# Kernel tuning notes

Hardware: AMD Instinct MI355X
Metric: run time of the kernel (lower is better)

Reference implementation:

```python
import jax, jax.numpy as jnp
import numpy as np

PS = 7        # pooled_size == conved_size
IMG = 300     # img_size
FMAP = 19     # feature map spatial size
SMAX = IMG // 16  # clamp max (18), matches torch long clamp(0, 300/16)
EPS = 1e-5


def _bn(x, g, b, m, v):
    scale = (g * jax.lax.rsqrt(v + EPS))[None, :, None, None]
    return x * scale + (b - m * g * jax.lax.rsqrt(v + EPS))[None, :, None, None]


def _conv(x, W, b=None, pad=1):
    y = jax.lax.conv_general_dilated(x, W, (1, 1), [(pad, pad), (pad, pad)],
                                     dimension_numbers=('NCHW', 'OIHW', 'NCHW'))
    if b is not None:
        y = y + b[None, :, None, None]
    return y


def _adaptive_w(lo, hi):
    # Per-ROI adaptive-avg-pool weights over the full 19-wide axis.
    # lo, hi: [B,R] inclusive crop bounds. Returns [B,R,PS,FMAP].
    H = hi - lo + 1                                  # crop length per ROI
    i = jnp.arange(PS)
    s = (i[None, None, :] * H[..., None]) // PS      # bin start (floor)
    e = -((-(i[None, None, :] + 1) * H[..., None]) // PS)  # bin end (ceil)
    rows = jnp.arange(FMAP)
    start = lo[..., None, None] + s[..., None]
    stop = lo[..., None, None] + e[..., None]
    mask = (rows >= start) & (rows < stop)
    denom = jnp.maximum(e - s, 1).astype(jnp.float32)[..., None]
    return mask.astype(jnp.float32) / denom


def setup_inputs() -> dict:
    key = jax.random.key(0)
    ks = jax.random.split(key, 6)
    B, R = 8, 128
    return {
        'roi_proposal': jax.random.uniform(ks[0], (B, 1, R, 5), dtype=jnp.float32),
        'features': jax.random.normal(ks[1], (B, 1024, FMAP, FMAP), dtype=jnp.float32),
        'W1': jax.random.normal(ks[2], (256, 1024, 3, 3), dtype=jnp.float32) * 0.02,
        'b1': jnp.zeros((256,), jnp.float32),
        'g1': jnp.ones((256,), jnp.float32),
        'be1': jnp.zeros((256,), jnp.float32),
        'm1': jnp.zeros((256,), jnp.float32),
        'v1': jnp.ones((256,), jnp.float32),
        'W2': jax.random.normal(ks[3], (256, 256, 3, 3), jnp.float32) * 0.05,
        'b2': jnp.zeros((256,), jnp.float32),
        'g2': jnp.ones((256,), jnp.float32),
        'be2': jnp.zeros((256,), jnp.float32),
        'm2': jnp.zeros((256,), jnp.float32),
        'v2': jnp.ones((256,), jnp.float32),
        'W3': jax.random.normal(ks[4], (32, 256, 1, 1), jnp.float32) * 0.1,
        'g3': jnp.ones((32,), jnp.float32),
        'be3': jnp.zeros((32,), jnp.float32),
        'm3': jnp.zeros((32,), jnp.float32),
        'v3': jnp.ones((32,), jnp.float32),
    }


def reference(roi_proposal, features, W1, b1, g1, be1, m1, v1,
              W2, b2, g2, be2, m2, v2, W3, g3, be3, m3, v3):
    # rois[..., 1:] * img_size / 16, then trunc to long (coords are >= 0)
    rl = (roi_proposal[:, 0, :, 1:] * (IMG / 16.0)).astype(jnp.int32)  # [B,R,4]
    c = jnp.clip(rl, 0, SMAX)
    xmin, ymin, xmax, ymax = c[..., 0], c[..., 1], c[..., 2], c[..., 3]
    valid = (xmax > xmin) & (ymax > ymin)                              # [B,R]
    B, R = valid.shape

    # fused crop + adaptive avg pool as two small pooling matmuls per ROI
    Wy = _adaptive_w(ymin, ymax)   # [B,R,7,19]
    Wx = _adaptive_w(xmin, xmax)   # [B,R,7,19]
    pooled = jnp.einsum('brph,bchw,brqw->brcpq', Wy, features, Wx)     # [B,R,1024,7,7]

    x = pooled.reshape(B * R, 1024, PS, PS)
    x = jax.nn.relu(_bn(_conv(x, W1, b1), g1, be1, m1, v1))
    x = jax.nn.relu(_bn(_conv(x, W2, b2), g2, be2, m2, v2))
    x = jax.nn.relu(_bn(_conv(x, W3, None, pad=0), g3, be3, m3, v3))
    out = x.reshape(B, R, 32, PS, PS) * valid[:, :, None, None, None]

    # compact valid ROIs to the front per batch (stable), invalid slots zeroed
    perm = jnp.argsort((~valid).astype(jnp.int32), axis=1, stable=True)
    out_c = jax.vmap(lambda o, p: o[p])(out, perm)                     # [B,R,32,7,7]
    er = rl.astype(jnp.float32) * (16.0 / IMG) * valid[..., None]
    er_c = jax.vmap(lambda o, p: o[p])(er, perm)[:, None]              # [B,1,R,4]
    keep_count = valid.sum(axis=1).astype(jnp.int32)                   # [B]
    return er_c, out_c, keep_count
```

## Files before the change

### kernel.cpp

```cpp
#include <hip/hip_runtime.h>
#include <cstddef>
#include <cstdint>

typedef unsigned short u16;
typedef unsigned int u32;
typedef __attribute__((ext_vector_type(8))) short short8;
typedef __attribute__((ext_vector_type(4))) float f32x4;

#define NB 8
#define NR 128
#define NPOS 49
#define EPSV 1e-5f
#define NSLOT 512

#define OUT_OC   4096
#define OUT_KEEP 1609728

static constexpr size_t OFF_META = 256;
static constexpr size_t OFF_KEEP = 33024;
static constexpr size_t OFF_W1Q  = 40960;
static constexpr size_t OFF_W2Q  = OFF_W1Q + 4718592;
static constexpr size_t OFF_W3   = OFF_W2Q + 1179648;
static constexpr size_t OFF_X1S  = OFF_W3  + 32768;
static constexpr size_t OFF_AP   = OFF_X1S + 13107200;
static constexpr size_t WS_NEED  = OFF_AP  + 51380224;

static __device__ __forceinline__ u16 f2bf(float f) {
  union { float f; u32 u; } x; x.f = f;
  u32 r = 0x7fffu + ((x.u >> 16) & 1u);
  return (u16)((x.u + r) >> 16);
}

__device__ __forceinline__ void int_body(const float* __restrict__ feat, float* __restrict__ S,
                                         int b, int cg, float* F)
{
  int tid = threadIdx.x;
  const float* fb = feat + ((size_t)b * 1024 + cg * 64) * 361;
#pragma unroll 1
  for (int i = tid; i < 64 * 361; i += 256) F[i] = fb[i];
  __syncthreads();
  if (tid < 64) {
    int ch = tid;
    const float* fp = F + ch * 361;
    float* Sp = S + (size_t)b * 400 * 1024 + cg * 64 + ch;
    float prev[20];
#pragma unroll
    for (int w = 0; w < 20; ++w) { prev[w] = 0.f; Sp[(size_t)w * 1024] = 0.f; }
    for (int h = 0; h < 19; ++h) {
      float run = 0.f;
      float* Sr = Sp + (size_t)(h + 1) * 20 * 1024;
      Sr[0] = 0.f;
#pragma unroll
      for (int w = 0; w < 19; ++w) {
        run += fp[h * 19 + w];
        float v = run + prev[w + 1];
        Sr[(size_t)(w + 1) * 1024] = v;
        prev[w + 1] = v;
      }
    }
  }
}

__device__ __forceinline__ void packw_body(const float* __restrict__ W, u16* __restrict__ wq,
                                           int IC, int c, int og, float* F)
{
  int tid = threadIdx.x, oc0 = og * 32;
#pragma unroll 1
  for (int i = tid; i < 18432; i += 256) {
    int ocr = i / 576, r = i - ocr * 576;
    F[i] = W[(size_t)(oc0 + ocr) * IC * 9 + c * 576 + r];
  }
  __syncthreads();
#pragma unroll 1
  for (int w = tid; w < 18432; w += 256) {
    int j = w & 7, lane = (w >> 3) & 63, rest = w >> 9;
    int ntr = rest & 1, kk = rest >> 1;
    int k9i = kk >> 1, ks = kk & 1;
    int ocr = ntr * 16 + (lane & 15);
    int icr = ks * 32 + ((lane >> 4) & 3) * 8 + j;
    int bid_ = (c * 9 + k9i) * 2 + ks;
    wq[((size_t)bid_ * 1024 + (oc0 / 16 + ntr) * 64 + lane) * 8 + j] = f2bf(F[ocr * 576 + icr * 9 + k9i]);
  }
}

__global__ __launch_bounds__(256) void k_prep(
    const float* __restrict__ feat, float* __restrict__ S,
    const float* __restrict__ W1, const float* __restrict__ W2, const float* __restrict__ W3,
    u16* __restrict__ w1q, u16* __restrict__ w2q, u16* __restrict__ w3q,
    const float* __restrict__ roi, int* __restrict__ cnt,
    int* __restrict__ meta, int* __restrict__ keepd, float* __restrict__ out)
{
  __shared__ float SH[23104];
  int bx = blockIdx.x;
  if (bx < 128) { int_body(feat, S, bx >> 4, bx & 15, SH); return; }
  if (bx < 256) { packw_body(W1, w1q, 1024, (bx - 128) >> 3, (bx - 128) & 7, SH); return; }
  if (bx < 288) { packw_body(W2, w2q, 256, (bx - 256) >> 3, (bx - 256) & 7, SH); return; }
  if (bx == 288) {
    for (int i = threadIdx.x; i < 8192; i += 256) {
      int oc = i >> 8, ic = i & 255;
      int kk = ic >> 5;
      int lane = ((ic >> 3) & 3) * 16 + (oc & 15);
      int nt16 = oc >> 4;
      int j = ic & 7;
      w3q[((size_t)((kk * 2 + nt16) * 64) + lane) * 8 + j] = f2bf(W3[i]);
    }
    return;
  }
  int b = bx - 289, t = threadIdx.x;
  int* sval = (int*)SH;
  int* spre = sval + 128;
  int rl[4], cl[4], valid = 0;
  if (t < 128) {
    const float* rp = roi + (size_t)(b * NR + t) * 5;
#pragma unroll
    for (int j = 0; j < 4; ++j) {
      rl[j] = (int)(rp[1 + j] * 18.75f);
      cl[j] = min(max(rl[j], 0), 18);
    }
    valid = (cl[2] > cl[0]) && (cl[3] > cl[1]) ? 1 : 0;
    sval[t] = valid;
  }
  __syncthreads();
  if (t == 0) {
    int s = 0;
    for (int i = 0; i < 128; ++i) { spre[i] = s; s += sval[i]; }
    spre[128] = s;
    keepd[b] = s;
    out[OUT_KEEP + b] = (float)s;
  }
  __syncthreads();
  if (t < 128) {
    int keep = spre[128];
    if (valid) {
      int dst = spre[t];
      int slot = atomicAdd(cnt, 1);
      int* mt = meta + slot * 8;
      mt[0] = b; mt[1] = dst;
      mt[2] = cl[1]; mt[3] = cl[3];
      mt[4] = cl[0]; mt[5] = cl[2];
#pragma unroll
      for (int j = 0; j < 4; ++j)
        out[(size_t)(b * NR + dst) * 4 + j] = (float)rl[j] * (16.0f / 300.0f);
    }
    if (t >= keep) {
#pragma unroll
      for (int j = 0; j < 4; ++j) out[(size_t)(b * NR + t) * 4 + j] = 0.f;
    }
  }
}

__global__ __launch_bounds__(256) void k_pool(
    const int* __restrict__ cnt, const int* __restrict__ meta,
    const float* __restrict__ S, u16* __restrict__ Apool)
{
  int cv = *cnt; if (cv > NSLOT) cv = NSLOT;
  int slot = blockIdx.x;
  if (slot >= cv) return;
  const int* mt_ = meta + slot * 8;
  int b = mt_[0], ylo = mt_[2], yhi = mt_[3], xlo = mt_[4], xhi = mt_[5];
  int Hy = yhi - ylo + 1, Hx = xhi - xlo + 1;
  const float* Sb = S + (size_t)b * 400 * 1024;
  u16* Ap = Apool + (size_t)slot * 50176;
  int base = blockIdx.y * 25088, end = base + 25088;
  int tid = threadIdx.x;
#pragma unroll 1
  for (int t0 = base + tid; t0 < end; t0 += 1024) {
#pragma unroll
    for (int u = 0; u < 4; ++u) {
      int t = t0 + u * 256;
      if (t < end) {
        int ch = t & 63, r = t >> 6;
        int bin = r % 49, c = r / 49;
        int p = bin / 7, q = bin - 7 * p;
        int sy = (p * Hy) / 7, ey = ((p + 1) * Hy + 6) / 7;
        int sx = (q * Hx) / 7, ex = ((q + 1) * Hx + 6) / 7;
        int y0 = ylo + sy, y1 = ylo + ey, x0 = xlo + sx, x1 = xlo + ex;
        const float* Sc = Sb + c * 64 + ch;
        float v = Sc[(size_t)(y1 * 20 + x1) * 1024] - Sc[(size_t)(y0 * 20 + x1) * 1024]
                - Sc[(size_t)(y1 * 20 + x0) * 1024] + Sc[(size_t)(y0 * 20 + x0) * 1024];
        v /= (float)((ey - sy) * (ex - sx));
        Ap[(size_t)c * 3136 + bin * 64 + ch] = f2bf(v);
      }
    }
  }
}

template<int STR>
__device__ __forceinline__ void build_aoffp(int n, int kq, int (&aoffp)[9][2]) {
#pragma unroll
  for (int t9 = 0; t9 < 9; ++t9) {
    int off[4];
#pragma unroll
    for (int mt = 0; mt < 4; ++mt) {
      int lm = mt * 16 + n;
      int mv = lm < 49;
      int lm2 = mv ? lm : 0;
      int p = lm2 / 7, q = lm2 - 7 * p;
      int ky = t9 / 3, kx = t9 - 3 * (t9 / 3);
      int ry = p + ky - 1, rx = q + kx - 1;
      int ok = mv && ry >= 0 && ry < 7 && rx >= 0 && rx < 7;
      int rr = ok ? ry * 7 + rx : 49;
      off[mt] = rr * STR + kq * 8;
    }
    aoffp[t9][0] = (off[0] & 0xFFFF) | (off[1] << 16);
    aoffp[t9][1] = (off[2] & 0xFFFF) | (off[3] << 16);
  }
}

__global__ __launch_bounds__(512) void k_conv1(
    const int* __restrict__ cnt, const u16* __restrict__ Apool, const u16* __restrict__ wq,
    const float* __restrict__ bb, const float* __restrict__ gg, const float* __restrict__ bec,
    const float* __restrict__ mm, const float* __restrict__ vv,
    u16* __restrict__ x1)
{
  int cv = *cnt; if (cv > NSLOT) cv = NSLOT;
  int slot0 = blockIdx.x * 4, ocq = blockIdx.y;
  if (slot0 >= cv) return;

  __shared__ __align__(16) u16 panels[8 * 3600];
  float* red = (float*)panels;

  int tid = threadIdx.x, lane = tid & 63, wave = tid >> 6;
  int kh = wave >> 2, roi4 = wave & 3;
  int n = lane & 15, kq = lane >> 4;

  for (int i = tid; i < 8 * 36; i += 512) {
    int sp = i / 36, w2 = i - sp * 36;
    ((u32*)(panels + sp * 3600 + 49 * 72))[w2] = 0;
  }

  int aoffp[9][2];
  build_aoffp<72>(n, kq, aoffp);
  f32x4 acc[4][4];
#pragma unroll
  for (int i = 0; i < 4; ++i)
#pragma unroll
    for (int j = 0; j < 4; ++j) acc[i][j] = (f32x4){0.f, 0.f, 0.f, 0.f};

  const u16* pf = wq + (size_t)(ocq * 4) * 512 + (size_t)lane * 8 + (size_t)(kh * 8) * 18 * 8192;
  short8 bbuf[2][4];
#pragma unroll
  for (int nt = 0; nt < 4; ++nt) bbuf[0][nt] = *(const short8*)(pf + nt * 512);
#pragma unroll
  for (int nt = 0; nt < 4; ++nt) bbuf[1][nt] = *(const short8*)(pf + 8192 + nt * 512);
  pf += (size_t)2 * 8192;

  auto stage = [&](int ca, int cb) {
#pragma unroll 1
    for (int t = tid; t < 3136; t += 512) {
      int khs = t >= 1568 ? 1 : 0;
      int e2 = t - khs * 1568;
      int rr = e2 / 392, e = e2 - rr * 392;
      int c = khs ? cb : ca;
      int sl = slot0 + rr; if (sl >= cv) sl = cv - 1;
      uint4 v = *((const uint4*)(Apool + ((size_t)sl * 16 + c) * 3136) + e);
      *(uint4*)(panels + (size_t)(khs * 4 + rr) * 3600 + (e >> 3) * 72 + (e & 7) * 8) = v;
    }
  };

  stage(0, 8);
  __syncthreads();

  const u16* P = panels + (size_t)(kh * 4 + roi4) * 3600;
#pragma unroll 1
  for (int i = 0; i < 8; ++i) {
#pragma unroll
    for (int kk = 0; kk < 18; ++kk) {
      int t9 = kk >> 1, ks = kk & 1;
      short8 bfr[4], afr[4];
#pragma unroll
      for (int nt = 0; nt < 4; ++nt) bfr[nt] = bbuf[kk & 1][nt];
#pragma unroll
      for (int nt = 0; nt < 4; ++nt) bbuf[kk & 1][nt] = *(const short8*)(pf + nt * 512);
      pf += 8192;
      int coff = ks * 32;
      int o0 = (aoffp[t9][0] & 0xFFFF) + coff, o1 = (int)((u32)aoffp[t9][0] >> 16) + coff;
      int o2 = (aoffp[t9][1] & 0xFFFF) + coff, o3 = (int)((u32)aoffp[t9][1] >> 16) + coff;
      afr[0] = *(const short8*)(P + o0); afr[1] = *(const short8*)(P + o1);
      afr[2] = *(const short8*)(P + o2); afr[3] = *(const short8*)(P + o3);
#pragma unroll
      for (int mt = 0; mt < 4; ++mt)
#pragma unroll
        for (int nt = 0; nt < 4; ++nt)
          acc[mt][nt] = __builtin_amdgcn_mfma_f32_16x16x32_bf16(afr[mt], bfr[nt], acc[mt][nt], 0, 0, 0);
    }
    __syncthreads();
    if (i + 1 < 8) {
      stage(i + 1, 9 + i);
      __syncthreads();
    }
  }

  if (kh == 1) {
#pragma unroll
    for (int nt = 0; nt < 4; ++nt)
#pragma unroll
      for (int mt = 0; mt < 4; ++mt)
#pragma unroll
        for (int r = 0; r < 4; ++r) {
          int m = mt * 16 + kq * 4 + r;
          if (m < 49) red[((size_t)roi4 * 49 + m) * 64 + nt * 16 + n] = acc[mt][nt][r];
        }
  }
  __syncthreads();
  if (kh == 0) {
    int slot = slot0 + roi4;
    if (slot < cv) {
#pragma unroll
      for (int nt = 0; nt < 4; ++nt) {
        int oc = ocq * 64 + nt * 16 + n;
        float sc = gg[oc] * rsqrtf(vv[oc] + EPSV);
        float sh = (bb[oc] - mm[oc]) * sc + bec[oc];
#pragma unroll
        for (int mt = 0; mt < 4; ++mt)
#pragma unroll
          for (int r = 0; r < 4; ++r) {
            int m = mt * 16 + kq * 4 + r;
            if (m < 49) {
              float y = acc[mt][nt][r] + red[((size_t)roi4 * 49 + m) * 64 + nt * 16 + n];
              y = fmaf(y, sc, sh);
              x1[((size_t)slot * 4 + ocq) * 3136 + m * 64 + nt * 16 + n] = f2bf(y > 0.f ? y : 0.f);
            }
          }
      }
    }
  }
}

__global__ __launch_bounds__(512) void k_conv23(
    const int* __restrict__ cnt, const int* __restrict__ meta, const int* __restrict__ keepd,
    const u16* __restrict__ x1, const u16* __restrict__ w2q, const u16* __restrict__ w3q,
    const float* __restrict__ b2, const float* __restrict__ g2, const float* __restrict__ be2,
    const float* __restrict__ m2, const float* __restrict__ v2,
    const float* __restrict__ g3, const float* __restrict__ be3,
    const float* __restrict__ m3, const float* __restrict__ v3,
    float* __restrict__ out)
{
  int cv = *cnt; if (cv > NSLOT) cv = NSLOT;
  int slot = blockIdx.x;
  int tid = threadIdx.x;
  if (slot >= cv) {
    int nfill = NSLOT - cv;
#pragma unroll 1
    for (int j = slot - cv; j < 1024; j += nfill) {
      int b = j >> 7, dd = j & 127;
      if (dd >= keepd[b]) {
        float* o = out + OUT_OC + (size_t)(b * NR + dd) * 1568;
        for (int t = tid; t < 1568; t += 512) o[t] = 0.f;
      }
    }
    return;
  }
  const int* mt_ = meta + slot * 8;
  int b = mt_[0], dst = mt_[1];

  __shared__ __align__(16) char smem[77600];
  u16*   panels = (u16*)smem;
  float* red    = (float*)smem;
  u16*   xp     = (u16*)(smem + 51200);
  float* red3   = (float*)smem;

  int lane = tid & 63, wave = tid >> 6;
  int nt4 = wave & 3, kh = wave >> 2;
  int n = lane & 15, kq = lane >> 4;

  for (int i = tid; i < 4 * 36; i += 512) {
    int sp = i / 36, w2 = i - sp * 36;
    ((u32*)(panels + sp * 3600 + 49 * 72))[w2] = 0;
  }
  const u16* xs = x1 + (size_t)slot * 4 * 3136;
#pragma unroll 1
  for (int t = tid; t < 1568; t += 512) {
    int c = t / 392, e = t - c * 392;
    uint4 v = *((const uint4*)(xs + (size_t)c * 3136) + e);
    *(uint4*)(panels + (size_t)c * 3600 + (e >> 3) * 72 + (e & 7) * 8) = v;
  }

  int aoffp[9][2];
  build_aoffp<72>(n, kq, aoffp);
  f32x4 acc[4][4];
#pragma unroll
  for (int i = 0; i < 4; ++i)
#pragma unroll
    for (int j = 0; j < 4; ++j) acc[i][j] = (f32x4){0.f, 0.f, 0.f, 0.f};

  const u16* pf = w2q + (size_t)(nt4 * 4) * 512 + (size_t)lane * 8 + (size_t)(kh * 36) * 8192;
  short8 bbuf[3][4];
#pragma unroll
  for (int r2 = 0; r2 < 3; ++r2)
#pragma unroll
    for (int nt = 0; nt < 4; ++nt) bbuf[r2][nt] = *(const short8*)(pf + (size_t)r2 * 8192 + nt * 512);
  pf += (size_t)3 * 8192;

  __syncthreads();

#pragma unroll 1
  for (int ci = 0; ci < 2; ++ci) {
    const u16* P = panels + (size_t)(kh * 2 + ci) * 3600;
#pragma unroll
    for (int kk = 0; kk < 18; ++kk) {
      int t9 = kk >> 1, ks = kk & 1;
      short8 bfr[4], afr[4];
#pragma unroll
      for (int nt = 0; nt < 4; ++nt) bfr[nt] = bbuf[kk % 3][nt];
#pragma unroll
      for (int nt = 0; nt < 4; ++nt) bbuf[kk % 3][nt] = *(const short8*)(pf + nt * 512);
      pf += 8192;
      int coff = ks * 32;
      int o0 = (aoffp[t9][0] & 0xFFFF) + coff, o1 = (int)((u32)aoffp[t9][0] >> 16) + coff;
      int o2 = (aoffp[t9][1] & 0xFFFF) + coff, o3 = (int)((u32)aoffp[t9][1] >> 16) + coff;
      afr[0] = *(const short8*)(P + o0); afr[1] = *(const short8*)(P + o1);
      afr[2] = *(const short8*)(P + o2); afr[3] = *(const short8*)(P + o3);
#pragma unroll
      for (int mt = 0; mt < 4; ++mt)
#pragma unroll
        for (int nt = 0; nt < 4; ++nt)
          acc[mt][nt] = __builtin_amdgcn_mfma_f32_16x16x32_bf16(afr[mt], bfr[nt], acc[mt][nt], 0, 0, 0);
    }
  }
  __syncthreads();

  if (kh == 1) {
#pragma unroll
    for (int nt = 0; nt < 4; ++nt)
#pragma unroll
      for (int mt = 0; mt < 4; ++mt)
#pragma unroll
        for (int r = 0; r < 4; ++r) {
          int m = mt * 16 + kq * 4 + r;
          if (m < 49) red[((size_t)nt4 * 49 + m) * 64 + nt * 16 + n] = acc[mt][nt][r];
        }
  }
  __syncthreads();
  if (kh == 0) {
#pragma unroll
    for (int nt = 0; nt < 4; ++nt) {
      int oc = nt4 * 64 + nt * 16 + n;
      float sc = g2[oc] * rsqrtf(v2[oc] + EPSV);
      float sh = (b2[oc] - m2[oc]) * sc + be2[oc];
#pragma unroll
      for (int mt = 0; mt < 4; ++mt)
#pragma unroll
        for (int r = 0; r < 4; ++r) {
          int m = mt * 16 + kq * 4 + r;
          if (m < 49) {
            float y = acc[mt][nt][r] + red[((size_t)nt4 * 49 + m) * 64 + nt * 16 + n];
            y = fmaf(y, sc, sh);
            xp[m * 264 + oc] = f2bf(y > 0.f ? y : 0.f);
          }
        }
    }
  }
  if (wave == 4) {
    for (int i = lane; i < 132; i += 64) ((u32*)(xp + 49 * 264))[i] = 0;
  }
  __syncthreads();

  f32x4 a3[4][2];
#pragma unroll
  for (int mt = 0; mt < 4; ++mt) { a3[mt][0] = (f32x4){0,0,0,0}; a3[mt][1] = (f32x4){0,0,0,0}; }
  const u16* b3 = w3q + ((size_t)(wave * 2) * 64 + lane) * 8;
  short8 bf0 = *(const short8*)(b3);
  short8 bf1 = *(const short8*)(b3 + 512);
#pragma unroll
  for (int mt = 0; mt < 4; ++mt) {
    int m = mt * 16 + n;
    int row = m < 49 ? m : 49;
    short8 a = *(const short8*)(xp + row * 264 + wave * 32 + kq * 8);
    a3[mt][0] = __builtin_amdgcn_mfma_f32_16x16x32_bf16(a, bf0, a3[mt][0], 0, 0, 0);
    a3[mt][1] = __builtin_amdgcn_mfma_f32_16x16x32_bf16(a, bf1, a3[mt][1], 0, 0, 0);
  }
#pragma unroll
  for (int nt = 0; nt < 2; ++nt)
#pragma unroll
    for (int mt = 0; mt < 4; ++mt)
#pragma unroll
      for (int r = 0; r < 4; ++r) {
        int m = mt * 16 + kq * 4 + r;
        if (m < 49) red3[((size_t)wave * 49 + m) * 32 + nt * 16 + n] = a3[mt][nt][r];
      }
  __syncthreads();

  size_t ob = OUT_OC + ((size_t)(b * NR + dst) * 32) * 49;
#pragma unroll 1
  for (int t = tid; t < 1568; t += 512) {
    int m = t >> 5, oc = t & 31;
    float s = 0.f;
#pragma unroll
    for (int w8 = 0; w8 < 8; ++w8) s += red3[((size_t)w8 * 49 + m) * 32 + oc];
    float sc = g3[oc] * rsqrtf(v3[oc] + EPSV);
    float y = fmaf(s, sc, be3[oc] - m3[oc] * sc);
    out[ob + (size_t)oc * 49 + m] = y > 0.f ? y : 0.f;
  }
}

extern "C" void kernel_launch(void* const* d_in, const int* in_sizes, int n_in,
                              void* d_out, int out_size, void* d_ws, size_t ws_size,
                              hipStream_t stream)
{
  (void)in_sizes; (void)n_in; (void)out_size;
  if (ws_size < WS_NEED) return;

  const float* roi  = (const float*)d_in[0];
  const float* feat = (const float*)d_in[1];
  const float* W1   = (const float*)d_in[2];
  const float* b1   = (const float*)d_in[3];
  const float* g1   = (const float*)d_in[4];
  const float* be1  = (const float*)d_in[5];
  const float* m1   = (const float*)d_in[6];
  const float* v1   = (const float*)d_in[7];
  const float* W2   = (const float*)d_in[8];
  const float* b2   = (const float*)d_in[9];
  const float* g2   = (const float*)d_in[10];
  const float* be2  = (const float*)d_in[11];
  const float* m2   = (const float*)d_in[12];
  const float* v2   = (const float*)d_in[13];
  const float* W3   = (const float*)d_in[14];
  const float* g3   = (const float*)d_in[15];
  const float* be3  = (const float*)d_in[16];
  const float* m3   = (const float*)d_in[17];
  const float* v3   = (const float*)d_in[18];

  char* ws    = (char*)d_ws;
  int*  cnt   = (int*)ws;
  int*  meta  = (int*)(ws + OFF_META);
  int*  keepd = (int*)(ws + OFF_KEEP);
  u16*  w1q   = (u16*)(ws + OFF_W1Q);
  u16*  w2q   = (u16*)(ws + OFF_W2Q);
  u16*  w3q   = (u16*)(ws + OFF_W3);
  float* S    = (float*)(ws + OFF_X1S);
  u16*  x1    = (u16*)(ws + OFF_X1S);
  u16*  Apool = (u16*)(ws + OFF_AP);
  float* out  = (float*)d_out;

  hipMemsetAsync(cnt, 0, 4, stream);

  k_prep<<<297, 256, 0, stream>>>(feat, S, W1, W2, W3, w1q, w2q, w3q,
                                  roi, cnt, meta, keepd, out);
  k_pool<<<dim3(NSLOT, 2), 256, 0, stream>>>(cnt, meta, S, Apool);
  k_conv1<<<dim3(NSLOT / 4, 4), 512, 0, stream>>>(cnt, Apool, w1q, b1, g1, be1, m1, v1, x1);
  k_conv23<<<NSLOT, 512, 0, stream>>>(cnt, meta, keepd, x1, w2q, w3q,
                                      b2, g2, be2, m2, v2, g3, be3, m3, v3, out);
}
```

Measured before the change: 293.2 us.

## Split conv1 K-reduction across four wave groups with 1024-thread blocks

k_conv1 now launches 1024 threads per block and splits the input-channel reduction four ways instead of two. Each wave group handles a quarter of the K dimension over 4 outer iterations instead of 8, and partial sums are combined through a two-level LDS tree reduction. The goal is more in-flight MFMA work per block and a shorter serial K loop per wave. The cost is doubled LDS use (16 panels), which limits blocks per CU, plus extra reduction syncs and register pressure under the 1024-thread launch bound.

```diff
diff --git a/kernel.cpp b/kernel.cpp
--- a/kernel.cpp
+++ b/kernel.cpp
@@ -207,7 +207,7 @@
   }
 }
 
-__global__ __launch_bounds__(512) void k_conv1(
+__global__ __launch_bounds__(1024) void k_conv1(
     const int* __restrict__ cnt, const u16* __restrict__ Apool, const u16* __restrict__ wq,
     const float* __restrict__ bb, const float* __restrict__ gg, const float* __restrict__ bec,
     const float* __restrict__ mm, const float* __restrict__ vv,
@@ -217,14 +217,15 @@
   int slot0 = blockIdx.x * 4, ocq = blockIdx.y;
   if (slot0 >= cv) return;
 
-  __shared__ __align__(16) u16 panels[8 * 3600];
-  float* red = (float*)panels;
+  __shared__ __align__(16) u16 panels[16 * 3600];
+  float* red1 = (float*)panels;
+  float* red2 = (float*)(panels + 25088);
 
   int tid = threadIdx.x, lane = tid & 63, wave = tid >> 6;
-  int kh = wave >> 2, roi4 = wave & 3;
+  int wk = wave >> 2, roi4 = wave & 3;
   int n = lane & 15, kq = lane >> 4;
 
-  for (int i = tid; i < 8 * 36; i += 512) {
+  for (int i = tid; i < 16 * 36; i += 1024) {
     int sp = i / 36, w2 = i - sp * 36;
     ((u32*)(panels + sp * 3600 + 49 * 72))[w2] = 0;
   }
@@ -237,7 +238,7 @@
 #pragma unroll
     for (int j = 0; j < 4; ++j) acc[i][j] = (f32x4){0.f, 0.f, 0.f, 0.f};
 
-  const u16* pf = wq + (size_t)(ocq * 4) * 512 + (size_t)lane * 8 + (size_t)(kh * 8) * 18 * 8192;
+  const u16* pf = wq + (size_t)(ocq * 4) * 512 + (size_t)lane * 8 + (size_t)(wk * 4) * 18 * 8192;
   short8 bbuf[2][4];
 #pragma unroll
   for (int nt = 0; nt < 4; ++nt) bbuf[0][nt] = *(const short8*)(pf + nt * 512);
@@ -245,25 +246,24 @@
   for (int nt = 0; nt < 4; ++nt) bbuf[1][nt] = *(const short8*)(pf + 8192 + nt * 512);
   pf += (size_t)2 * 8192;
 
-  auto stage = [&](int ca, int cb) {
-#pragma unroll 1
-    for (int t = tid; t < 3136; t += 512) {
-      int khs = t >= 1568 ? 1 : 0;
-      int e2 = t - khs * 1568;
+  auto stage = [&](int i) {
+#pragma unroll 1
+    for (int t = tid; t < 6272; t += 1024) {
+      int kqs = t / 1568, e2 = t - kqs * 1568;
       int rr = e2 / 392, e = e2 - rr * 392;
-      int c = khs ? cb : ca;
+      int c = kqs * 4 + i;
       int sl = slot0 + rr; if (sl >= cv) sl = cv - 1;
       uint4 v = *((const uint4*)(Apool + ((size_t)sl * 16 + c) * 3136) + e);
-      *(uint4*)(panels + (size_t)(khs * 4 + rr) * 3600 + (e >> 3) * 72 + (e & 7) * 8) = v;
+      *(uint4*)(panels + (size_t)(kqs * 4 + rr) * 3600 + (e >> 3) * 72 + (e & 7) * 8) = v;
     }
   };
 
-  stage(0, 8);
-  __syncthreads();
-
-  const u16* P = panels + (size_t)(kh * 4 + roi4) * 3600;
-#pragma unroll 1
-  for (int i = 0; i < 8; ++i) {
+  stage(0);
+  __syncthreads();
+
+  const u16* P = panels + (size_t)(wk * 4 + roi4) * 3600;
+#pragma unroll 1
+  for (int i = 0; i < 4; ++i) {
 #pragma unroll
     for (int kk = 0; kk < 18; ++kk) {
       int t9 = kk >> 1, ks = kk & 1;
@@ -285,13 +285,14 @@
           acc[mt][nt] = __builtin_amdgcn_mfma_f32_16x16x32_bf16(afr[mt], bfr[nt], acc[mt][nt], 0, 0, 0);
     }
     __syncthreads();
-    if (i + 1 < 8) {
-      stage(i + 1, 9 + i);
+    if (i + 1 < 4) {
+      stage(i + 1);
       __syncthreads();
     }
   }
 
-  if (kh == 1) {
+  if (wk == 1 || wk == 3) {
+    float* rd = (wk == 1) ? red1 : red2;
 #pragma unroll
     for (int nt = 0; nt < 4; ++nt)
 #pragma unroll
@@ -299,11 +300,36 @@
 #pragma unroll
         for (int r = 0; r < 4; ++r) {
           int m = mt * 16 + kq * 4 + r;
-          if (m < 49) red[((size_t)roi4 * 49 + m) * 64 + nt * 16 + n] = acc[mt][nt][r];
+          if (m < 49) rd[((size_t)roi4 * 49 + m) * 64 + nt * 16 + n] = acc[mt][nt][r];
         }
   }
   __syncthreads();
-  if (kh == 0) {
+  if (wk == 0 || wk == 2) {
+    const float* rd = (wk == 0) ? red1 : red2;
+#pragma unroll
+    for (int nt = 0; nt < 4; ++nt)
+#pragma unroll
+      for (int mt = 0; mt < 4; ++mt)
+#pragma unroll
+        for (int r = 0; r < 4; ++r) {
+          int m = mt * 16 + kq * 4 + r;
+          if (m < 49) acc[mt][nt][r] += rd[((size_t)roi4 * 49 + m) * 64 + nt * 16 + n];
+        }
+  }
+  __syncthreads();
+  if (wk == 2) {
+#pragma unroll
+    for (int nt = 0; nt < 4; ++nt)
+#pragma unroll
+      for (int mt = 0; mt < 4; ++mt)
+#pragma unroll
+        for (int r = 0; r < 4; ++r) {
+          int m = mt * 16 + kq * 4 + r;
+          if (m < 49) red1[((size_t)roi4 * 49 + m) * 64 + nt * 16 + n] = acc[mt][nt][r];
+        }
+  }
+  __syncthreads();
+  if (wk == 0) {
     int slot = slot0 + roi4;
     if (slot < cv) {
 #pragma unroll
@@ -317,7 +343,7 @@
           for (int r = 0; r < 4; ++r) {
             int m = mt * 16 + kq * 4 + r;
             if (m < 49) {
-              float y = acc[mt][nt][r] + red[((size_t)roi4 * 49 + m) * 64 + nt * 16 + n];
+              float y = acc[mt][nt][r] + red1[((size_t)roi4 * 49 + m) * 64 + nt * 16 + n];
               y = fmaf(y, sc, sh);
               x1[((size_t)slot * 4 + ocq) * 3136 + m * 64 + nt * 16 + n] = f2bf(y > 0.f ? y : 0.f);
             }
@@ -538,7 +564,7 @@
   k_prep<<<297, 256, 0, stream>>>(feat, S, W1, W2, W3, w1q, w2q, w3q,
                                   roi, cnt, meta, keepd, out);
   k_pool<<<dim3(NSLOT, 2), 256, 0, stream>>>(cnt, meta, S, Apool);
-  k_conv1<<<dim3(NSLOT / 4, 4), 512, 0, stream>>>(cnt, Apool, w1q, b1, g1, be1, m1, v1, x1);
+  k_conv1<<<dim3(NSLOT / 4, 4), 1024, 0, stream>>>(cnt, Apool, w1q, b1, g1, be1, m1, v1, x1);
   k_conv23<<<NSLOT, 512, 0, stream>>>(cnt, meta, keepd, x1, w2q, w3q,
                                       b2, g2, be2, m2, v2, g3, be3, m3, v3, out);
 }
```

After: 286.4 us. 2.3% less time.
